# Kernel optimization log

Measured on AMD Instinct MI355X. Metric: run time of the kernel, lower is better.

Reference implementation:

```python
import jax, jax.numpy as jnp
import numpy as np

N_NODES = 50000
N_EDGES = 800000
F_IN = 128
F_OUT = 128


def gcn_conv(x, W, b, src, tgt, w, n):
    # x: [n, F_in]; GCNConv with add_self_loops=True, improved=False (fill=1.0)
    lin = x @ W  # [n, F_out]
    deg = jax.ops.segment_sum(w, tgt, num_segments=n) + 1.0  # self-loop weight 1
    dinv = jax.lax.rsqrt(deg)
    normw = dinv[src] * w * dinv[tgt]  # [E]
    agg = jax.ops.segment_sum(lin[src] * normw[:, None], tgt, num_segments=n)
    return agg + lin * (dinv * dinv)[:, None] + b


def setup_inputs() -> dict:
    key = jax.random.key(0)
    ks = jax.random.split(key, 16)
    X = jax.random.normal(ks[0], (1, N_NODES, F_IN), jnp.float32)
    edge_index = jax.random.randint(ks[1], (2, N_EDGES), 0, N_NODES, jnp.int64)
    edge_weight = jax.random.uniform(ks[2], (N_EDGES,), jnp.float32)
    H = jax.random.normal(ks[3], (1, N_NODES, F_OUT), jnp.float32)
    s = 1.0 / np.sqrt(F_IN)
    s2 = 1.0 / np.sqrt(2 * F_OUT)
    params = {
        'W_z': jax.random.uniform(ks[4], (F_IN, F_OUT), jnp.float32, -s, s),
        'b_z': jnp.zeros((F_OUT,), jnp.float32),
        'W_r': jax.random.uniform(ks[5], (F_IN, F_OUT), jnp.float32, -s, s),
        'b_r': jnp.zeros((F_OUT,), jnp.float32),
        'W_h': jax.random.uniform(ks[6], (F_IN, F_OUT), jnp.float32, -s, s),
        'b_h': jnp.zeros((F_OUT,), jnp.float32),
        'Wl_z': jax.random.uniform(ks[7], (2 * F_OUT, F_OUT), jnp.float32, -s2, s2),
        'bl_z': jax.random.uniform(ks[8], (F_OUT,), jnp.float32, -s2, s2),
        'Wl_r': jax.random.uniform(ks[9], (2 * F_OUT, F_OUT), jnp.float32, -s2, s2),
        'bl_r': jax.random.uniform(ks[10], (F_OUT,), jnp.float32, -s2, s2),
        'Wl_h': jax.random.uniform(ks[11], (2 * F_OUT, F_OUT), jnp.float32, -s2, s2),
        'bl_h': jax.random.uniform(ks[12], (F_OUT,), jnp.float32, -s2, s2),
    }
    return dict(X=X, edge_index=edge_index, edge_weight=edge_weight, H=H, **params)


def reference(X, edge_index, edge_weight, H,
              W_z, b_z, W_r, b_r, W_h, b_h,
              Wl_z, bl_z, Wl_r, bl_r, Wl_h, bl_h):
    B, N, _ = X.shape
    n = B * N
    x = X.reshape(n, -1)
    src, tgt = edge_index[0], edge_index[1]

    cz = gcn_conv(x, W_z, b_z, src, tgt, edge_weight, n).reshape(B, N, -1)
    Z = jax.nn.sigmoid(jnp.concatenate([cz, H], axis=2) @ Wl_z + bl_z)

    cr = gcn_conv(x, W_r, b_r, src, tgt, edge_weight, n).reshape(B, N, -1)
    R = jax.nn.sigmoid(jnp.concatenate([cr, H], axis=2) @ Wl_r + bl_r)

    ch = gcn_conv(x, W_h, b_h, src, tgt, edge_weight, n).reshape(B, N, -1)
    H_tilde = jnp.tanh(jnp.concatenate([ch, H * R], axis=2) @ Wl_h + bl_h)

    return Z * H + (1.0 - Z) * H_tilde
```

## Files before the change

kernel.cpp:

```cpp
#include <hip/hip_runtime.h>
#include <hip/hip_bf16.h>

#define N_NODES 50000
#define N_EDGES 800000
#define M_PAD   50048
#define NBLK5   1564
#define CAP     96

typedef __attribute__((ext_vector_type(8))) short bf16x8_t;
typedef __attribute__((ext_vector_type(4))) float f32x4_t;

__device__ __forceinline__ unsigned short f2bf(float f) {
    unsigned u = __float_as_uint(f);
    u += 0x7FFFu + ((u >> 16) & 1u);
    return (unsigned short)(u >> 16);
}
__device__ __forceinline__ float bf2f(unsigned short h) {
    return __uint_as_float(((unsigned)h) << 16);
}


__global__ void prep1_kernel(const float* __restrict__ Wz, const float* __restrict__ Wr,
                             const float* __restrict__ Wh,
                             const float* __restrict__ bz, const float* __restrict__ br,
                             const float* __restrict__ bh,
                             const float* __restrict__ Wlz, const float* __restrict__ Wlr,
                             const float* __restrict__ Wlh,
                             const float* __restrict__ blz, const float* __restrict__ blr,
                             const float* __restrict__ blh,
                             float* __restrict__ Pf, float* __restrict__ cg,
                             int* __restrict__ counts) {
    int tid = blockIdx.x * 256 + threadIdx.x;
    if (tid < N_NODES) counts[tid] = 0;
    if (tid < 3 * 16384) {
        int g = tid / 16384, k = (tid / 128) % 128, n = tid & 127;
        const float* W  = (g == 0) ? Wz  : (g == 1) ? Wr  : Wh;
        const float* Wl = (g == 0) ? Wlz : (g == 1) ? Wlr : Wlh;
        float acc = 0.f;
        #pragma unroll 8
        for (int j = 0; j < 128; ++j)
            acc = fmaf(W[k * 128 + j], Wl[j * 128 + n], acc);
        Pf[tid] = acc;
    } else if (tid < 3 * 16384 + 384) {
        int u = tid - 3 * 16384;
        int g = u / 128, n = u & 127;
        const float* b  = (g == 0) ? bz  : (g == 1) ? br  : bh;
        const float* Wl = (g == 0) ? Wlz : (g == 1) ? Wlr : Wlh;
        const float* bl = (g == 0) ? blz : (g == 1) ? blr : blh;
        float acc = bl[n];
        #pragma unroll 8
        for (int j = 0; j < 128; ++j)
            acc = fmaf(b[j], Wl[j * 128 + n], acc);
        cg[u] = acc;
    }
}

__global__ void wfrag2_kernel(const float* __restrict__ Pf,
                              const float* __restrict__ Wlz, const float* __restrict__ Wlr,
                              const float* __restrict__ Wlh,
                              unsigned short* __restrict__ Wf2) {
    int tid = blockIdx.x * 256 + threadIdx.x;
    if (tid >= 6 * 2048) return;
    int m = tid / 2048, t = tid % 2048;
    int nt = t / 256, ks = (t / 64) % 4, lane = t % 64;
    const float* src;
    if (m < 3) src = Pf + m * 16384;
    else       src = ((m == 3) ? Wlz : (m == 4) ? Wlr : Wlh) + 128 * 128;
    unsigned short* dst = Wf2 + m * 16384 + ((nt * 4 + ks) * 64 + lane) * 8;
    int n = nt * 16 + (lane & 15);
    int k0 = ks * 32 + 8 * (lane >> 4);
    #pragma unroll
    for (int j = 0; j < 8; ++j) dst[j] = f2bf(src[(k0 + j) * 128 + n]);
}

__global__ void place_kernel(const int* __restrict__ EI, const float* __restrict__ EW,
                             int* __restrict__ counts, int2* __restrict__ rec,
                             const float* __restrict__ Hf, unsigned short* __restrict__ Hb) {
    int i = blockIdx.x * 256 + threadIdx.x;
    if (i < N_NODES * 32) {
        float4 h = ((const float4*)Hf)[i];
        ushort4 b;
        b.x = f2bf(h.x); b.y = f2bf(h.y); b.z = f2bf(h.z); b.w = f2bf(h.w);
        ((ushort4*)Hb)[i] = b;
    }
    if (i < N_EDGES) {
        int s = EI[i];
        int t = EI[N_EDGES + i];
        int pos = atomicAdd(&counts[t], 1);
        if (pos < CAP) rec[(size_t)t * CAP + pos] = make_int2(s, __float_as_int(EW[i]));
    }
}

__global__ void deg_kernel(const int* __restrict__ counts, const int2* __restrict__ rec,
                           float* __restrict__ dinv) {
    int n = blockIdx.x * 256 + threadIdx.x;
    if (n >= N_NODES) return;
    int c = counts[n]; c = (c < CAP) ? c : CAP;
    const int2* rb = rec + (size_t)n * CAP;
    float d = 1.0f;
    #pragma unroll 4
    for (int e = 0; e < c; ++e) d += __int_as_float(rb[e].y);
    dinv[n] = rsqrtf(d);
}

__global__ void convert_kernel(const float* __restrict__ X, const float* __restrict__ dinv,
                               unsigned short* __restrict__ Xb) {
    int i = blockIdx.x * 256 + threadIdx.x;
    if (i >= N_NODES * 32) return;
    int node = i >> 5;
    float di = dinv[node];
    float4 x = ((const float4*)X)[i];
    ushort4 a;
    a.x = f2bf(di * x.x); a.y = f2bf(di * x.y); a.z = f2bf(di * x.z); a.w = f2bf(di * x.w);
    ((ushort4*)Xb)[i] = a;
}


__global__ __launch_bounds__(256) void fused_kernel(const unsigned short* __restrict__ Xb,
                                                    const unsigned short* __restrict__ Hb,
                                                    const float* __restrict__ Hf,
                                                    const float* __restrict__ dinv,
                                                    const int* __restrict__ counts,
                                                    const int2* __restrict__ rec,
                                                    const unsigned short* __restrict__ Wf2,
                                                    const float* __restrict__ cg,
                                                    float* __restrict__ out) {
    __shared__ unsigned short ys[32][136];
    __shared__ unsigned short rls[32][136];
    int wave = threadIdx.x >> 6, lane = threadIdx.x & 63;
    int rowbase = blockIdx.x * 32;
    int rlo = lane & 15;
    int kg = 8 * (lane >> 4);
    int n0 = wave * 2;

    {
        int grp = lane >> 3, lg = lane & 7;
        int nl = wave * 8 + grp;
        int node = rowbase + nl;
        if (node < N_NODES) {
            float acc[16];
            {
                bf16x8_t x0 = *(const bf16x8_t*)(Xb + (size_t)node * 128 + lg * 16);
                bf16x8_t x1 = *(const bf16x8_t*)(Xb + (size_t)node * 128 + lg * 16 + 8);
                #pragma unroll
                for (int j = 0; j < 8; ++j) {
                    acc[j] = bf2f((unsigned short)x0[j]);
                    acc[8 + j] = bf2f((unsigned short)x1[j]);
                }
            }
            int c = counts[node]; c = (c < CAP) ? c : CAP;
            const int2* rb = rec + (size_t)node * CAP;
            int e = 0;
            int2 r;
            bf16x8_t xa0, xa1;
            float wcur = 0.f;
            if (e < c) {
                r = rb[0];
                xa0 = *(const bf16x8_t*)(Xb + (size_t)r.x * 128 + lg * 16);
                xa1 = *(const bf16x8_t*)(Xb + (size_t)r.x * 128 + lg * 16 + 8);
                wcur = __int_as_float(r.y);
                if (1 < c) r = rb[1];
            }
            while (e < c) {
                bf16x8_t xb0, xb1;
                float wn = 0.f;
                int en = e + 1;
                if (en < c) {
                    xb0 = *(const bf16x8_t*)(Xb + (size_t)r.x * 128 + lg * 16);
                    xb1 = *(const bf16x8_t*)(Xb + (size_t)r.x * 128 + lg * 16 + 8);
                    wn = __int_as_float(r.y);
                    if (en + 1 < c) r = rb[en + 1];
                }
                #pragma unroll
                for (int j = 0; j < 8; ++j) {
                    acc[j] = fmaf(wcur, bf2f((unsigned short)xa0[j]), acc[j]);
                    acc[8 + j] = fmaf(wcur, bf2f((unsigned short)xa1[j]), acc[8 + j]);
                }
                xa0 = xb0; xa1 = xb1; wcur = wn;
                e = en;
            }
            float dt = dinv[node];
            ushort4 o0, o1, o2, o3;
            o0.x = f2bf(dt * acc[0]);  o0.y = f2bf(dt * acc[1]);
            o0.z = f2bf(dt * acc[2]);  o0.w = f2bf(dt * acc[3]);
            o1.x = f2bf(dt * acc[4]);  o1.y = f2bf(dt * acc[5]);
            o1.z = f2bf(dt * acc[6]);  o1.w = f2bf(dt * acc[7]);
            o2.x = f2bf(dt * acc[8]);  o2.y = f2bf(dt * acc[9]);
            o2.z = f2bf(dt * acc[10]); o2.w = f2bf(dt * acc[11]);
            o3.x = f2bf(dt * acc[12]); o3.y = f2bf(dt * acc[13]);
            o3.z = f2bf(dt * acc[14]); o3.w = f2bf(dt * acc[15]);
            *(ushort4*)(&ys[nl][lg * 16])      = o0;
            *(ushort4*)(&ys[nl][lg * 16 + 4])  = o1;
            *(ushort4*)(&ys[nl][lg * 16 + 8])  = o2;
            *(ushort4*)(&ys[nl][lg * 16 + 12]) = o3;
        } else {
            ushort4 z = {0, 0, 0, 0};
            *(ushort4*)(&ys[nl][lg * 16])      = z;
            *(ushort4*)(&ys[nl][lg * 16 + 4])  = z;
            *(ushort4*)(&ys[nl][lg * 16 + 8])  = z;
            *(ushort4*)(&ys[nl][lg * 16 + 12]) = z;
        }
    }
    __syncthreads();

    const unsigned short* Az = Wf2;
    const unsigned short* Ar = Wf2 + 16384;
    const unsigned short* Ah = Wf2 + 2 * 16384;
    const unsigned short* Bz = Wf2 + 3 * 16384;
    const unsigned short* Br = Wf2 + 4 * 16384;
    const unsigned short* Bh = Wf2 + 5 * 16384;
    const float* cz = cg;
    const float* cr = cg + 128;
    const float* ch = cg + 256;

    bf16x8_t ay[2][4], ah[2][4];
    #pragma unroll
    for (int rt = 0; rt < 2; ++rt) {
        int r0 = rowbase + rt * 16 + rlo;
        #pragma unroll
        for (int ks = 0; ks < 4; ++ks) {
            ay[rt][ks] = *(const bf16x8_t*)(&ys[rt * 16 + rlo][ks * 32 + kg]);
            ah[rt][ks] = *(const bf16x8_t*)(Hb + (size_t)r0 * 128 + ks * 32 + kg);
        }
    }

    {
        f32x4_t acc[2][2];
        #pragma unroll
        for (int rt = 0; rt < 2; ++rt)
            #pragma unroll
            for (int c = 0; c < 2; ++c) acc[rt][c] = f32x4_t{0.f, 0.f, 0.f, 0.f};
        #pragma unroll
        for (int ks = 0; ks < 4; ++ks) {
            bf16x8_t b0 = *(const bf16x8_t*)(Ar + (((n0 + 0) * 4 + ks) * 64 + lane) * 8);
            bf16x8_t b1 = *(const bf16x8_t*)(Ar + (((n0 + 1) * 4 + ks) * 64 + lane) * 8);
            acc[0][0] = __builtin_amdgcn_mfma_f32_16x16x32_bf16(ay[0][ks], b0, acc[0][0], 0, 0, 0);
            acc[1][0] = __builtin_amdgcn_mfma_f32_16x16x32_bf16(ay[1][ks], b0, acc[1][0], 0, 0, 0);
            acc[0][1] = __builtin_amdgcn_mfma_f32_16x16x32_bf16(ay[0][ks], b1, acc[0][1], 0, 0, 0);
            acc[1][1] = __builtin_amdgcn_mfma_f32_16x16x32_bf16(ay[1][ks], b1, acc[1][1], 0, 0, 0);
        }
        #pragma unroll
        for (int ks = 0; ks < 4; ++ks) {
            bf16x8_t b0 = *(const bf16x8_t*)(Br + (((n0 + 0) * 4 + ks) * 64 + lane) * 8);
            bf16x8_t b1 = *(const bf16x8_t*)(Br + (((n0 + 1) * 4 + ks) * 64 + lane) * 8);
            acc[0][0] = __builtin_amdgcn_mfma_f32_16x16x32_bf16(ah[0][ks], b0, acc[0][0], 0, 0, 0);
            acc[1][0] = __builtin_amdgcn_mfma_f32_16x16x32_bf16(ah[1][ks], b0, acc[1][0], 0, 0, 0);
            acc[0][1] = __builtin_amdgcn_mfma_f32_16x16x32_bf16(ah[0][ks], b1, acc[0][1], 0, 0, 0);
            acc[1][1] = __builtin_amdgcn_mfma_f32_16x16x32_bf16(ah[1][ks], b1, acc[1][1], 0, 0, 0);
        }
        #pragma unroll
        for (int c = 0; c < 2; ++c) {
            int col = (n0 + c) * 16 + rlo;
            float crv = cr[col];
            #pragma unroll
            for (int rt = 0; rt < 2; ++rt)
                #pragma unroll
                for (int r = 0; r < 4; ++r) {
                    float pv = acc[rt][c][r] + crv;
                    float rv = 1.0f / (1.0f + __expf(-pv));
                    rls[rt * 16 + 4 * (lane >> 4) + r][col] = f2bf(rv);
                }
        }
        __syncthreads();
    }

    {
        f32x4_t az[2][2], ath[2][2];
        #pragma unroll
        for (int rt = 0; rt < 2; ++rt)
            #pragma unroll
            for (int c = 0; c < 2; ++c) {
                az[rt][c] = f32x4_t{0.f, 0.f, 0.f, 0.f};
                ath[rt][c] = f32x4_t{0.f, 0.f, 0.f, 0.f};
            }
        #pragma unroll
        for (int ks = 0; ks < 4; ++ks) {
            bf16x8_t bz0 = *(const bf16x8_t*)(Az + (((n0 + 0) * 4 + ks) * 64 + lane) * 8);
            bf16x8_t bz1 = *(const bf16x8_t*)(Az + (((n0 + 1) * 4 + ks) * 64 + lane) * 8);
            bf16x8_t bh0 = *(const bf16x8_t*)(Ah + (((n0 + 0) * 4 + ks) * 64 + lane) * 8);
            bf16x8_t bh1 = *(const bf16x8_t*)(Ah + (((n0 + 1) * 4 + ks) * 64 + lane) * 8);
            az[0][0]  = __builtin_amdgcn_mfma_f32_16x16x32_bf16(ay[0][ks], bz0, az[0][0], 0, 0, 0);
            az[1][0]  = __builtin_amdgcn_mfma_f32_16x16x32_bf16(ay[1][ks], bz0, az[1][0], 0, 0, 0);
            az[0][1]  = __builtin_amdgcn_mfma_f32_16x16x32_bf16(ay[0][ks], bz1, az[0][1], 0, 0, 0);
            az[1][1]  = __builtin_amdgcn_mfma_f32_16x16x32_bf16(ay[1][ks], bz1, az[1][1], 0, 0, 0);
            ath[0][0] = __builtin_amdgcn_mfma_f32_16x16x32_bf16(ay[0][ks], bh0, ath[0][0], 0, 0, 0);
            ath[1][0] = __builtin_amdgcn_mfma_f32_16x16x32_bf16(ay[1][ks], bh0, ath[1][0], 0, 0, 0);
            ath[0][1] = __builtin_amdgcn_mfma_f32_16x16x32_bf16(ay[0][ks], bh1, ath[0][1], 0, 0, 0);
            ath[1][1] = __builtin_amdgcn_mfma_f32_16x16x32_bf16(ay[1][ks], bh1, ath[1][1], 0, 0, 0);
        }
        #pragma unroll
        for (int ks = 0; ks < 4; ++ks) {
            bf16x8_t hr0, hr1;
            {
                bf16x8_t rf0 = *(const bf16x8_t*)(&rls[rlo][ks * 32 + kg]);
                bf16x8_t rf1 = *(const bf16x8_t*)(&rls[16 + rlo][ks * 32 + kg]);
                #pragma unroll
                for (int j = 0; j < 8; ++j) {
                    hr0[j] = (short)f2bf(bf2f((unsigned short)ah[0][ks][j]) * bf2f((unsigned short)rf0[j]));
                    hr1[j] = (short)f2bf(bf2f((unsigned short)ah[1][ks][j]) * bf2f((unsigned short)rf1[j]));
                }
            }
            bf16x8_t bz0 = *(const bf16x8_t*)(Bz + (((n0 + 0) * 4 + ks) * 64 + lane) * 8);
            bf16x8_t bz1 = *(const bf16x8_t*)(Bz + (((n0 + 1) * 4 + ks) * 64 + lane) * 8);
            bf16x8_t bh0 = *(const bf16x8_t*)(Bh + (((n0 + 0) * 4 + ks) * 64 + lane) * 8);
            bf16x8_t bh1 = *(const bf16x8_t*)(Bh + (((n0 + 1) * 4 + ks) * 64 + lane) * 8);
            az[0][0]  = __builtin_amdgcn_mfma_f32_16x16x32_bf16(ah[0][ks], bz0, az[0][0], 0, 0, 0);
            az[1][0]  = __builtin_amdgcn_mfma_f32_16x16x32_bf16(ah[1][ks], bz0, az[1][0], 0, 0, 0);
            az[0][1]  = __builtin_amdgcn_mfma_f32_16x16x32_bf16(ah[0][ks], bz1, az[0][1], 0, 0, 0);
            az[1][1]  = __builtin_amdgcn_mfma_f32_16x16x32_bf16(ah[1][ks], bz1, az[1][1], 0, 0, 0);
            ath[0][0] = __builtin_amdgcn_mfma_f32_16x16x32_bf16(hr0, bh0, ath[0][0], 0, 0, 0);
            ath[1][0] = __builtin_amdgcn_mfma_f32_16x16x32_bf16(hr1, bh0, ath[1][0], 0, 0, 0);
            ath[0][1] = __builtin_amdgcn_mfma_f32_16x16x32_bf16(hr0, bh1, ath[0][1], 0, 0, 0);
            ath[1][1] = __builtin_amdgcn_mfma_f32_16x16x32_bf16(hr1, bh1, ath[1][1], 0, 0, 0);
        }
        #pragma unroll
        for (int c = 0; c < 2; ++c) {
            int col = (n0 + c) * 16 + rlo;
            float czv = cz[col];
            float chv = ch[col];
            #pragma unroll
            for (int rt = 0; rt < 2; ++rt)
                #pragma unroll
                for (int r = 0; r < 4; ++r) {
                    int row = rowbase + rt * 16 + 4 * (lane >> 4) + r;
                    if (row < N_NODES) {
                        float pz = az[rt][c][r] + czv;
                        float z = 1.0f / (1.0f + __expf(-pz));
                        float ph = ath[rt][c][r] + chv;
                        float t = __expf(-2.0f * fabsf(ph));
                        float th = (1.0f - t) / (1.0f + t);
                        th = copysignf(th, ph);
                        float h = Hf[(size_t)row * 128 + col];
                        out[(size_t)row * 128 + col] = z * h + (1.0f - z) * th;
                    }
                }
        }
    }
}


extern "C" void kernel_launch(void* const* d_in, const int* in_sizes, int n_in,
                              void* d_out, int out_size, void* d_ws, size_t ws_size,
                              hipStream_t stream) {
    const float*      X   = (const float*)d_in[0];
    const int*        EI  = (const int*)d_in[1];
    const float*      EW  = (const float*)d_in[2];
    const float*      Hf  = (const float*)d_in[3];
    const float*      Wz  = (const float*)d_in[4];
    const float*      bz  = (const float*)d_in[5];
    const float*      Wr  = (const float*)d_in[6];
    const float*      br  = (const float*)d_in[7];
    const float*      Wh  = (const float*)d_in[8];
    const float*      bh  = (const float*)d_in[9];
    const float*      Wlz = (const float*)d_in[10];
    const float*      blz = (const float*)d_in[11];
    const float*      Wlr = (const float*)d_in[12];
    const float*      blr = (const float*)d_in[13];
    const float*      Wlh = (const float*)d_in[14];
    const float*      blh = (const float*)d_in[15];
    float* out = (float*)d_out;

    char* p = (char*)d_ws;
    auto alloc = [&](size_t bytes) {
        char* r = p;
        p += (bytes + 255) & ~(size_t)255;
        return r;
    };
    int*   counts = (int*)alloc(M_PAD * 4);
    float* dinv   = (float*)alloc(M_PAD * 4);
    int2*  rec    = (int2*)alloc((size_t)N_NODES * CAP * 8);
    unsigned short* Xb  = (unsigned short*)alloc((size_t)M_PAD * 128 * 2);
    unsigned short* Hb  = (unsigned short*)alloc((size_t)M_PAD * 128 * 2);
    float* Pf  = (float*)alloc(3 * 128 * 128 * 4);
    float* cgb = (float*)alloc(3 * 128 * 4);
    unsigned short* Wf2 = (unsigned short*)alloc(6 * 128 * 128 * 2);

    prep1_kernel<<<196, 256, 0, stream>>>(Wz, Wr, Wh, bz, br, bh,
                                          Wlz, Wlr, Wlh, blz, blr, blh,
                                          Pf, cgb, counts);
    wfrag2_kernel<<<48, 256, 0, stream>>>(Pf, Wlz, Wlr, Wlh, Wf2);
    place_kernel<<<6250, 256, 0, stream>>>(EI, EW, counts, rec, Hf, Hb);
    deg_kernel<<<196, 256, 0, stream>>>(counts, rec, dinv);
    convert_kernel<<<6250, 256, 0, stream>>>(X, dinv, Xb);
    fused_kernel<<<NBLK5, 256, 0, stream>>>(Xb, Hb, Hf, dinv, counts, rec, Wf2, cgb, out);
}
```

Before: 151.3 us.

## Double threads per block, split edge gather across lane halves, stage H in LDS

The fused kernel now runs 512 threads per block. Each node's edge list is split between two 8-lane halves that take alternating edges, and the partial sums are combined with a cross-lane shuffle, doubling gather parallelism per node. Each wave now computes one 16-column tile instead of two. H is staged once as bf16 in shared memory and reused both for the MFMA inputs and for the final blend, replacing the fp32 H reads from global memory. This adds a shuffle reduction and more LDS traffic, and the final blend now uses bf16-rounded H instead of fp32, which is a precision loss.

```diff
diff --git a/kernel.cpp b/kernel.cpp
--- a/kernel.cpp
+++ b/kernel.cpp
@@ -116,9 +116,8 @@
 }
 
 
-__global__ __launch_bounds__(256) void fused_kernel(const unsigned short* __restrict__ Xb,
+__global__ __launch_bounds__(512) void fused_kernel(const unsigned short* __restrict__ Xb,
                                                     const unsigned short* __restrict__ Hb,
-                                                    const float* __restrict__ Hf,
                                                     const float* __restrict__ dinv,
                                                     const int* __restrict__ counts,
                                                     const int2* __restrict__ rec,
@@ -126,20 +125,37 @@
                                                     const float* __restrict__ cg,
                                                     float* __restrict__ out) {
     __shared__ unsigned short ys[32][136];
+    __shared__ unsigned short hs[32][136];
     __shared__ unsigned short rls[32][136];
-    int wave = threadIdx.x >> 6, lane = threadIdx.x & 63;
+    int tid = threadIdx.x;
+    int wave = tid >> 6, lane = tid & 63;
     int rowbase = blockIdx.x * 32;
     int rlo = lane & 15;
     int kg = 8 * (lane >> 4);
-    int n0 = wave * 2;
+    int n0 = wave;
 
     {
-        int grp = lane >> 3, lg = lane & 7;
-        int nl = wave * 8 + grp;
+        int r = tid >> 4, co = (tid & 15) * 8;
+        int row = rowbase + r;
+        bf16x8_t h;
+        if (row < N_NODES) h = *(const bf16x8_t*)(Hb + (size_t)row * 128 + co);
+        else {
+            #pragma unroll
+            for (int j = 0; j < 8; ++j) h[j] = 0;
+        }
+        *(bf16x8_t*)(&hs[r][co]) = h;
+    }
+
+    {
+        int nl = wave * 4 + (lane >> 4);
+        int half = (lane >> 3) & 1;
+        int lg = lane & 7;
         int node = rowbase + nl;
+        float acc[16];
+        #pragma unroll
+        for (int j = 0; j < 16; ++j) acc[j] = 0.f;
         if (node < N_NODES) {
-            float acc[16];
-            {
+            if (half == 0) {
                 bf16x8_t x0 = *(const bf16x8_t*)(Xb + (size_t)node * 128 + lg * 16);
                 bf16x8_t x1 = *(const bf16x8_t*)(Xb + (size_t)node * 128 + lg * 16 + 8);
                 #pragma unroll
@@ -150,26 +166,26 @@
             }
             int c = counts[node]; c = (c < CAP) ? c : CAP;
             const int2* rb = rec + (size_t)node * CAP;
-            int e = 0;
+            int e = half;
             int2 r;
             bf16x8_t xa0, xa1;
             float wcur = 0.f;
             if (e < c) {
-                r = rb[0];
+                r = rb[e];
                 xa0 = *(const bf16x8_t*)(Xb + (size_t)r.x * 128 + lg * 16);
                 xa1 = *(const bf16x8_t*)(Xb + (size_t)r.x * 128 + lg * 16 + 8);
                 wcur = __int_as_float(r.y);
-                if (1 < c) r = rb[1];
+                if (e + 2 < c) r = rb[e + 2];
             }
             while (e < c) {
                 bf16x8_t xb0, xb1;
                 float wn = 0.f;
-                int en = e + 1;
+                int en = e + 2;
                 if (en < c) {
                     xb0 = *(const bf16x8_t*)(Xb + (size_t)r.x * 128 + lg * 16);
                     xb1 = *(const bf16x8_t*)(Xb + (size_t)r.x * 128 + lg * 16 + 8);
                     wn = __int_as_float(r.y);
-                    if (en + 1 < c) r = rb[en + 1];
+                    if (en + 2 < c) r = rb[en + 2];
                 }
                 #pragma unroll
                 for (int j = 0; j < 8; ++j) {
@@ -179,7 +195,11 @@
                 xa0 = xb0; xa1 = xb1; wcur = wn;
                 e = en;
             }
-            float dt = dinv[node];
+        }
+        #pragma unroll
+        for (int j = 0; j < 16; ++j) acc[j] += __shfl_xor(acc[j], 8, 64);
+        if (half == 0) {
+            float dt = (node < N_NODES) ? dinv[node] : 0.f;
             ushort4 o0, o1, o2, o3;
             o0.x = f2bf(dt * acc[0]);  o0.y = f2bf(dt * acc[1]);
             o0.z = f2bf(dt * acc[2]);  o0.w = f2bf(dt * acc[3]);
@@ -193,12 +213,6 @@
             *(ushort4*)(&ys[nl][lg * 16 + 4])  = o1;
             *(ushort4*)(&ys[nl][lg * 16 + 8])  = o2;
             *(ushort4*)(&ys[nl][lg * 16 + 12]) = o3;
-        } else {
-            ushort4 z = {0, 0, 0, 0};
-            *(ushort4*)(&ys[nl][lg * 16])      = z;
-            *(ushort4*)(&ys[nl][lg * 16 + 4])  = z;
-            *(ushort4*)(&ys[nl][lg * 16 + 8])  = z;
-            *(ushort4*)(&ys[nl][lg * 16 + 12]) = z;
         }
     }
     __syncthreads();
@@ -209,131 +223,92 @@
     const unsigned short* Bz = Wf2 + 3 * 16384;
     const unsigned short* Br = Wf2 + 4 * 16384;
     const unsigned short* Bh = Wf2 + 5 * 16384;
-    const float* cz = cg;
-    const float* cr = cg + 128;
-    const float* ch = cg + 256;
-
-    bf16x8_t ay[2][4], ah[2][4];
-    #pragma unroll
-    for (int rt = 0; rt < 2; ++rt) {
-        int r0 = rowbase + rt * 16 + rlo;
+    int col = n0 * 16 + rlo;
+
+    {
+        f32x4_t a0 = f32x4_t{0.f, 0.f, 0.f, 0.f};
+        f32x4_t a1 = f32x4_t{0.f, 0.f, 0.f, 0.f};
         #pragma unroll
         for (int ks = 0; ks < 4; ++ks) {
-            ay[rt][ks] = *(const bf16x8_t*)(&ys[rt * 16 + rlo][ks * 32 + kg]);
-            ah[rt][ks] = *(const bf16x8_t*)(Hb + (size_t)r0 * 128 + ks * 32 + kg);
-        }
-    }
+            bf16x8_t y0 = *(const bf16x8_t*)(&ys[rlo][ks * 32 + kg]);
+            bf16x8_t y1 = *(const bf16x8_t*)(&ys[16 + rlo][ks * 32 + kg]);
+            bf16x8_t b = *(const bf16x8_t*)(Ar + ((n0 * 4 + ks) * 64 + lane) * 8);
+            a0 = __builtin_amdgcn_mfma_f32_16x16x32_bf16(y0, b, a0, 0, 0, 0);
+            a1 = __builtin_amdgcn_mfma_f32_16x16x32_bf16(y1, b, a1, 0, 0, 0);
+        }
+        #pragma unroll
+        for (int ks = 0; ks < 4; ++ks) {
+            bf16x8_t h0 = *(const bf16x8_t*)(&hs[rlo][ks * 32 + kg]);
+            bf16x8_t h1 = *(const bf16x8_t*)(&hs[16 + rlo][ks * 32 + kg]);
+            bf16x8_t b = *(const bf16x8_t*)(Br + ((n0 * 4 + ks) * 64 + lane) * 8);
+            a0 = __builtin_amdgcn_mfma_f32_16x16x32_bf16(h0, b, a0, 0, 0, 0);
+            a1 = __builtin_amdgcn_mfma_f32_16x16x32_bf16(h1, b, a1, 0, 0, 0);
+        }
+        float crv = cg[128 + col];
+        #pragma unroll
+        for (int r = 0; r < 4; ++r) {
+            float p0 = a0[r] + crv;
+            float p1 = a1[r] + crv;
+            rls[4 * (lane >> 4) + r][col] = f2bf(1.0f / (1.0f + __expf(-p0)));
+            rls[16 + 4 * (lane >> 4) + r][col] = f2bf(1.0f / (1.0f + __expf(-p1)));
+        }
+    }
+    __syncthreads();
 
     {
-        f32x4_t acc[2][2];
-        #pragma unroll
-        for (int rt = 0; rt < 2; ++rt)
+        f32x4_t az0 = f32x4_t{0.f, 0.f, 0.f, 0.f};
+        f32x4_t az1 = f32x4_t{0.f, 0.f, 0.f, 0.f};
+        f32x4_t at0 = f32x4_t{0.f, 0.f, 0.f, 0.f};
+        f32x4_t at1 = f32x4_t{0.f, 0.f, 0.f, 0.f};
+        #pragma unroll
+        for (int ks = 0; ks < 4; ++ks) {
+            bf16x8_t y0 = *(const bf16x8_t*)(&ys[rlo][ks * 32 + kg]);
+            bf16x8_t y1 = *(const bf16x8_t*)(&ys[16 + rlo][ks * 32 + kg]);
+            bf16x8_t bz_ = *(const bf16x8_t*)(Az + ((n0 * 4 + ks) * 64 + lane) * 8);
+            bf16x8_t bh_ = *(const bf16x8_t*)(Ah + ((n0 * 4 + ks) * 64 + lane) * 8);
+            az0 = __builtin_amdgcn_mfma_f32_16x16x32_bf16(y0, bz_, az0, 0, 0, 0);
+            az1 = __builtin_amdgcn_mfma_f32_16x16x32_bf16(y1, bz_, az1, 0, 0, 0);
+            at0 = __builtin_amdgcn_mfma_f32_16x16x32_bf16(y0, bh_, at0, 0, 0, 0);
+            at1 = __builtin_amdgcn_mfma_f32_16x16x32_bf16(y1, bh_, at1, 0, 0, 0);
+        }
+        #pragma unroll
+        for (int ks = 0; ks < 4; ++ks) {
+            bf16x8_t h0 = *(const bf16x8_t*)(&hs[rlo][ks * 32 + kg]);
+            bf16x8_t h1 = *(const bf16x8_t*)(&hs[16 + rlo][ks * 32 + kg]);
+            bf16x8_t rf0 = *(const bf16x8_t*)(&rls[rlo][ks * 32 + kg]);
+            bf16x8_t rf1 = *(const bf16x8_t*)(&rls[16 + rlo][ks * 32 + kg]);
+            bf16x8_t hr0, hr1;
             #pragma unroll
-            for (int c = 0; c < 2; ++c) acc[rt][c] = f32x4_t{0.f, 0.f, 0.f, 0.f};
-        #pragma unroll
-        for (int ks = 0; ks < 4; ++ks) {
-            bf16x8_t b0 = *(const bf16x8_t*)(Ar + (((n0 + 0) * 4 + ks) * 64 + lane) * 8);
-            bf16x8_t b1 = *(const bf16x8_t*)(Ar + (((n0 + 1) * 4 + ks) * 64 + lane) * 8);
-            acc[0][0] = __builtin_amdgcn_mfma_f32_16x16x32_bf16(ay[0][ks], b0, acc[0][0], 0, 0, 0);
-            acc[1][0] = __builtin_amdgcn_mfma_f32_16x16x32_bf16(ay[1][ks], b0, acc[1][0], 0, 0, 0);
-            acc[0][1] = __builtin_amdgcn_mfma_f32_16x16x32_bf16(ay[0][ks], b1, acc[0][1], 0, 0, 0);
-            acc[1][1] = __builtin_amdgcn_mfma_f32_16x16x32_bf16(ay[1][ks], b1, acc[1][1], 0, 0, 0);
-        }
-        #pragma unroll
-        for (int ks = 0; ks < 4; ++ks) {
-            bf16x8_t b0 = *(const bf16x8_t*)(Br + (((n0 + 0) * 4 + ks) * 64 + lane) * 8);
-            bf16x8_t b1 = *(const bf16x8_t*)(Br + (((n0 + 1) * 4 + ks) * 64 + lane) * 8);
-            acc[0][0] = __builtin_amdgcn_mfma_f32_16x16x32_bf16(ah[0][ks], b0, acc[0][0], 0, 0, 0);
-            acc[1][0] = __builtin_amdgcn_mfma_f32_16x16x32_bf16(ah[1][ks], b0, acc[1][0], 0, 0, 0);
-            acc[0][1] = __builtin_amdgcn_mfma_f32_16x16x32_bf16(ah[0][ks], b1, acc[0][1], 0, 0, 0);
-            acc[1][1] = __builtin_amdgcn_mfma_f32_16x16x32_bf16(ah[1][ks], b1, acc[1][1], 0, 0, 0);
-        }
-        #pragma unroll
-        for (int c = 0; c < 2; ++c) {
-            int col = (n0 + c) * 16 + rlo;
-            float crv = cr[col];
+            for (int j = 0; j < 8; ++j) {
+                hr0[j] = (short)f2bf(bf2f((unsigned short)h0[j]) * bf2f((unsigned short)rf0[j]));
+                hr1[j] = (short)f2bf(bf2f((unsigned short)h1[j]) * bf2f((unsigned short)rf1[j]));
+            }
+            bf16x8_t bz_ = *(const bf16x8_t*)(Bz + ((n0 * 4 + ks) * 64 + lane) * 8);
+            bf16x8_t bh_ = *(const bf16x8_t*)(Bh + ((n0 * 4 + ks) * 64 + lane) * 8);
+            az0 = __builtin_amdgcn_mfma_f32_16x16x32_bf16(h0, bz_, az0, 0, 0, 0);
+            az1 = __builtin_amdgcn_mfma_f32_16x16x32_bf16(h1, bz_, az1, 0, 0, 0);
+            at0 = __builtin_amdgcn_mfma_f32_16x16x32_bf16(hr0, bh_, at0, 0, 0, 0);
+            at1 = __builtin_amdgcn_mfma_f32_16x16x32_bf16(hr1, bh_, at1, 0, 0, 0);
+        }
+        float czv = cg[col];
+        float chv = cg[256 + col];
+        #pragma unroll
+        for (int rt = 0; rt < 2; ++rt) {
             #pragma unroll
-            for (int rt = 0; rt < 2; ++rt)
-                #pragma unroll
-                for (int r = 0; r < 4; ++r) {
-                    float pv = acc[rt][c][r] + crv;
-                    float rv = 1.0f / (1.0f + __expf(-pv));
-                    rls[rt * 16 + 4 * (lane >> 4) + r][col] = f2bf(rv);
+            for (int r = 0; r < 4; ++r) {
+                int rl = rt * 16 + 4 * (lane >> 4) + r;
+                int row = rowbase + rl;
+                if (row < N_NODES) {
+                    float pz = (rt == 0 ? az0[r] : az1[r]) + czv;
+                    float z = 1.0f / (1.0f + __expf(-pz));
+                    float ph = (rt == 0 ? at0[r] : at1[r]) + chv;
+                    float t = __expf(-2.0f * fabsf(ph));
+                    float th = (1.0f - t) / (1.0f + t);
+                    th = copysignf(th, ph);
+                    float h = bf2f(hs[rl][col]);
+                    out[(size_t)row * 128 + col] = z * h + (1.0f - z) * th;
                 }
-        }
-        __syncthreads();
-    }
-
-    {
-        f32x4_t az[2][2], ath[2][2];
-        #pragma unroll
-        for (int rt = 0; rt < 2; ++rt)
-            #pragma unroll
-            for (int c = 0; c < 2; ++c) {
-                az[rt][c] = f32x4_t{0.f, 0.f, 0.f, 0.f};
-                ath[rt][c] = f32x4_t{0.f, 0.f, 0.f, 0.f};
-            }
-        #pragma unroll
-        for (int ks = 0; ks < 4; ++ks) {
-            bf16x8_t bz0 = *(const bf16x8_t*)(Az + (((n0 + 0) * 4 + ks) * 64 + lane) * 8);
-            bf16x8_t bz1 = *(const bf16x8_t*)(Az + (((n0 + 1) * 4 + ks) * 64 + lane) * 8);
-            bf16x8_t bh0 = *(const bf16x8_t*)(Ah + (((n0 + 0) * 4 + ks) * 64 + lane) * 8);
-            bf16x8_t bh1 = *(const bf16x8_t*)(Ah + (((n0 + 1) * 4 + ks) * 64 + lane) * 8);
-            az[0][0]  = __builtin_amdgcn_mfma_f32_16x16x32_bf16(ay[0][ks], bz0, az[0][0], 0, 0, 0);
-            az[1][0]  = __builtin_amdgcn_mfma_f32_16x16x32_bf16(ay[1][ks], bz0, az[1][0], 0, 0, 0);
-            az[0][1]  = __builtin_amdgcn_mfma_f32_16x16x32_bf16(ay[0][ks], bz1, az[0][1], 0, 0, 0);
-            az[1][1]  = __builtin_amdgcn_mfma_f32_16x16x32_bf16(ay[1][ks], bz1, az[1][1], 0, 0, 0);
-            ath[0][0] = __builtin_amdgcn_mfma_f32_16x16x32_bf16(ay[0][ks], bh0, ath[0][0], 0, 0, 0);
-            ath[1][0] = __builtin_amdgcn_mfma_f32_16x16x32_bf16(ay[1][ks], bh0, ath[1][0], 0, 0, 0);
-            ath[0][1] = __builtin_amdgcn_mfma_f32_16x16x32_bf16(ay[0][ks], bh1, ath[0][1], 0, 0, 0);
-            ath[1][1] = __builtin_amdgcn_mfma_f32_16x16x32_bf16(ay[1][ks], bh1, ath[1][1], 0, 0, 0);
-        }
-        #pragma unroll
-        for (int ks = 0; ks < 4; ++ks) {
-            bf16x8_t hr0, hr1;
-            {
-                bf16x8_t rf0 = *(const bf16x8_t*)(&rls[rlo][ks * 32 + kg]);
-                bf16x8_t rf1 = *(const bf16x8_t*)(&rls[16 + rlo][ks * 32 + kg]);
-                #pragma unroll
-                for (int j = 0; j < 8; ++j) {
-                    hr0[j] = (short)f2bf(bf2f((unsigned short)ah[0][ks][j]) * bf2f((unsigned short)rf0[j]));
-                    hr1[j] = (short)f2bf(bf2f((unsigned short)ah[1][ks][j]) * bf2f((unsigned short)rf1[j]));
-                }
-            }
-            bf16x8_t bz0 = *(const bf16x8_t*)(Bz + (((n0 + 0) * 4 + ks) * 64 + lane) * 8);
-            bf16x8_t bz1 = *(const bf16x8_t*)(Bz + (((n0 + 1) * 4 + ks) * 64 + lane) * 8);
-            bf16x8_t bh0 = *(const bf16x8_t*)(Bh + (((n0 + 0) * 4 + ks) * 64 + lane) * 8);
-            bf16x8_t bh1 = *(const bf16x8_t*)(Bh + (((n0 + 1) * 4 + ks) * 64 + lane) * 8);
-            az[0][0]  = __builtin_amdgcn_mfma_f32_16x16x32_bf16(ah[0][ks], bz0, az[0][0], 0, 0, 0);
-            az[1][0]  = __builtin_amdgcn_mfma_f32_16x16x32_bf16(ah[1][ks], bz0, az[1][0], 0, 0, 0);
-            az[0][1]  = __builtin_amdgcn_mfma_f32_16x16x32_bf16(ah[0][ks], bz1, az[0][1], 0, 0, 0);
-            az[1][1]  = __builtin_amdgcn_mfma_f32_16x16x32_bf16(ah[1][ks], bz1, az[1][1], 0, 0, 0);
-            ath[0][0] = __builtin_amdgcn_mfma_f32_16x16x32_bf16(hr0, bh0, ath[0][0], 0, 0, 0);
-            ath[1][0] = __builtin_amdgcn_mfma_f32_16x16x32_bf16(hr1, bh0, ath[1][0], 0, 0, 0);
-            ath[0][1] = __builtin_amdgcn_mfma_f32_16x16x32_bf16(hr0, bh1, ath[0][1], 0, 0, 0);
-            ath[1][1] = __builtin_amdgcn_mfma_f32_16x16x32_bf16(hr1, bh1, ath[1][1], 0, 0, 0);
-        }
-        #pragma unroll
-        for (int c = 0; c < 2; ++c) {
-            int col = (n0 + c) * 16 + rlo;
-            float czv = cz[col];
-            float chv = ch[col];
-            #pragma unroll
-            for (int rt = 0; rt < 2; ++rt)
-                #pragma unroll
-                for (int r = 0; r < 4; ++r) {
-                    int row = rowbase + rt * 16 + 4 * (lane >> 4) + r;
-                    if (row < N_NODES) {
-                        float pz = az[rt][c][r] + czv;
-                        float z = 1.0f / (1.0f + __expf(-pz));
-                        float ph = ath[rt][c][r] + chv;
-                        float t = __expf(-2.0f * fabsf(ph));
-                        float th = (1.0f - t) / (1.0f + t);
-                        th = copysignf(th, ph);
-                        float h = Hf[(size_t)row * 128 + col];
-                        out[(size_t)row * 128 + col] = z * h + (1.0f - z) * th;
-                    }
-                }
+            }
         }
     }
 }
@@ -382,5 +357,5 @@
     place_kernel<<<6250, 256, 0, stream>>>(EI, EW, counts, rec, Hf, Hb);
     deg_kernel<<<196, 256, 0, stream>>>(counts, rec, dinv);
     convert_kernel<<<6250, 256, 0, stream>>>(X, dinv, Xb);
-    fused_kernel<<<NBLK5, 256, 0, stream>>>(Xb, Hb, Hf, dinv, counts, rec, Wf2, cgb, out);
-}
+    fused_kernel<<<NBLK5, 512, 0, stream>>>(Xb, Hb, dinv, counts, rec, Wf2, cgb, out);
+}
```

Result: faster. 138.3 us (-8.6%).
